# Kernel tuning notes

Measured on AMD Instinct MI355X. Metric: run time of the kernel, lower is better.

The kernel has to match this reference:

```python
import jax, jax.numpy as jnp
import numpy as np

B, H, W, C, NH, WS = 4, 128, 128, 128, 4, 8
N = WS * WS
HD = C // NH
SCALE = HD ** -0.5
MLP_H = 4 * C


def _rel_index():
    coords = np.stack(np.meshgrid(np.arange(WS), np.arange(WS), indexing='ij'))
    flat = coords.reshape(2, -1)
    rel = (flat[:, :, None] - flat[:, None, :]).transpose(1, 2, 0).astype(np.int64)
    rel[..., 0] += WS - 1
    rel[..., 1] += WS - 1
    rel[..., 0] *= 2 * WS - 1
    return jnp.asarray(rel.sum(-1))  # (N, N)

REL_IDX = _rel_index()


def layer_norm(x, w, b):
    m = jnp.mean(x, -1, keepdims=True)
    v = jnp.mean((x - m) ** 2, -1, keepdims=True)
    return (x - m) * jax.lax.rsqrt(v + 1e-5) * w + b


def window_partition(x):  # (B, H*W, C) -> (B*nW, N, C)
    t = x.reshape(B, H // WS, WS, W // WS, WS, C).transpose(0, 1, 3, 2, 4, 5)
    return t.reshape(-1, N, C)


def window_reverse(wins):  # (B*nW, N, C) -> (B, H*W, C)
    t = wins.reshape(B, H // WS, W // WS, WS, WS, C).transpose(0, 1, 3, 2, 4, 5)
    return t.reshape(B, H * W, C)


def setup_inputs():
    key = jax.random.key(0)
    ks = jax.random.split(key, 8)
    rn = lambda k, s: jax.random.normal(k, s, jnp.float32) * 0.02
    return {
        'x': jax.random.normal(ks[0], (B, H * W, C), jnp.float32),
        'd': jax.random.normal(ks[1], (B, H * W, C), jnp.float32),
        'rpb_table': rn(ks[2], ((2 * WS - 1) ** 2, NH)),
        'norm1_w': jnp.ones((C,), jnp.float32), 'norm1_b': jnp.zeros((C,), jnp.float32),
        'norm2_w': jnp.ones((C,), jnp.float32), 'norm2_b': jnp.zeros((C,), jnp.float32),
        'qkv1_w': rn(ks[3], (4 * C, C)), 'qkv1_b': jnp.zeros((4 * C,), jnp.float32),
        'proj_w': rn(ks[4], (C, C)), 'proj_b': jnp.zeros((C,), jnp.float32),
        'fc1_w': rn(ks[5], (MLP_H, C)), 'fc1_b': jnp.zeros((MLP_H,), jnp.float32),
        'fc2_w': rn(ks[6], (C, MLP_H)), 'fc2_b': jnp.zeros((C,), jnp.float32),
    }


def _attn_core(xw, dw, rpb_table, qkv1_w, qkv1_b, proj_w, proj_b):
    def qkv(t):
        q = (t @ qkv1_w.T + qkv1_b).reshape(-1, N, 4, NH, HD)
        return jnp.moveaxis(q, 2, 0).transpose(0, 1, 3, 2, 4)  # (4, B_, NH, N, HD)

    q_r, k_r, v_r, q_rd = qkv(xw)
    q_d, k_d, v_d, q_dr = qkv(dw)
    bias = rpb_table[REL_IDX].transpose(2, 0, 1)  # (NH, N, N)
    sm = jax.nn.softmax
    dot = lambda q, k: jnp.einsum('bhnd,bhmd->bhnm', q * SCALE, k)
    attn = sm(dot(q_r, k_r) + bias[None])      # bias only on r-branch (as in torch)
    attn_rd = sm(dot(q_dr, k_r))
    attn_d = sm(dot(q_d, k_d))
    attn_dr = sm(dot(q_rd, k_d))
    av = lambda a, v: jnp.einsum('bhnm,bhmd->bhnd', a, v).transpose(0, 2, 1, 3).reshape(-1, N, C)
    x_out = av(attn, v_r) + av(attn_rd, v_r)
    d_out = av(attn_dr, v_d) + av(attn_d, v_d)
    return x_out @ proj_w.T + proj_b, d_out @ proj_w.T + proj_b


def reference(x, d, rpb_table, norm1_w, norm1_b, norm2_w, norm2_b, qkv1_w, qkv1_b, proj_w, proj_b, fc1_w, fc1_b, fc2_w, fc2_b):
    xw = window_partition(layer_norm(x, norm1_w, norm1_b))
    dw = window_partition(layer_norm(d, norm1_w, norm1_b))
    xa, da = _attn_core(xw, dw, rpb_table, qkv1_w, qkv1_b, proj_w, proj_b)
    x = x + window_reverse(xa)
    d = d + window_reverse(da)
    mlp = lambda t: jax.nn.gelu(t @ fc1_w.T + fc1_b, approximate=False) @ fc2_w.T + fc2_b
    x = x + mlp(layer_norm(x, norm2_w, norm2_b))
    d = d + mlp(layer_norm(d, norm2_w, norm2_b))
    return x, d
```

## Files before the change

kernel.cpp:

```cpp
#include <hip/hip_runtime.h>
#include <hip/hip_bf16.h>
#include <math.h>

typedef short bf16x8 __attribute__((ext_vector_type(8)));
typedef float f32x4 __attribute__((ext_vector_type(4)));

#define QKSCALE_L2E 0.25505402227437564f
#define LOG2E 1.4426950408889634f

__device__ __forceinline__ unsigned short f2bf(float f) {
  __hip_bfloat16 h = __float2bfloat16(f);
  return *reinterpret_cast<unsigned short*>(&h);
}
__device__ __forceinline__ unsigned int pk2(float lo, float hi) {
  __hip_bfloat162 h = __float22bfloat162_rn(make_float2(lo, hi));
  return *reinterpret_cast<unsigned int*>(&h);
}
__device__ __forceinline__ bf16x8 pack8(const float* g) {
  union { unsigned int u[4]; bf16x8 v; } t;
  t.u[0] = pk2(g[0], g[1]); t.u[1] = pk2(g[2], g[3]);
  t.u[2] = pk2(g[4], g[5]); t.u[3] = pk2(g[6], g[7]);
  return t.v;
}

__device__ __forceinline__ bf16x8 ldsv(const unsigned short* base, int row, int strideHalfs, int kHalf, int swzMask) {
  int byte = row * strideHalfs * 2 + kHalf * 2;
  byte ^= (row & swzMask) << 4;
  return *(const bf16x8*)((const char*)base + byte);
}
__device__ __forceinline__ void ldss(unsigned short* base, int row, int strideHalfs, int col, int swzMask, unsigned short v) {
  int byte = row * strideHalfs * 2 + col * 2;
  byte ^= (row & swzMask) << 4;
  *(unsigned short*)((char*)base + byte) = v;
}
__device__ __forceinline__ void ldst32(unsigned short* base, int row, int strideHalfs, int colHalf, int swzMask, unsigned int v) {
  int byte = row * strideHalfs * 2 + colHalf * 2;
  byte ^= (row & swzMask) << 4;
  *(unsigned int*)((char*)base + byte) = v;
}
__device__ __forceinline__ void ldst64(unsigned short* base, int row, int strideHalfs, int colHalf, int swzMask, unsigned int lo, unsigned int hi) {
  int byte = row * strideHalfs * 2 + colHalf * 2;
  byte ^= (row & swzMask) << 4;
  uint2 val; val.x = lo; val.y = hi;
  *(uint2*)((char*)base + byte) = val;
}

__global__ void prep_kernel(
    const float* __restrict__ qkv1_w, const float* __restrict__ qkv1_b,
    const float* __restrict__ proj_w, const float* __restrict__ fc1_w,
    const float* __restrict__ fc2_w,  const float* __restrict__ rpb,
    unsigned short* __restrict__ Wqkvf, unsigned short* __restrict__ Wprojf,
    unsigned short* __restrict__ Wfc1f, unsigned short* __restrict__ Wfc2f,
    float* __restrict__ bqkv, float* __restrict__ biasmat)
{
  int i = blockIdx.x * 256 + threadIdx.x;
  if (i < 65536) {
    int j = i & 7, lane = (i >> 3) & 63, kk = (i >> 9) & 3;
    int sub16 = (i >> 11) & 1, h = (i >> 12) & 3, comp = i >> 14;
    int row = comp * 128 + h * 32 + sub16 * 16 + (lane & 15);
    int col = kk * 32 + (lane >> 4) * 8 + j;
    float sc = (comp == 0 || comp == 3) ? QKSCALE_L2E : 1.f;
    Wqkvf[i] = f2bf(qkv1_w[row * 128 + col] * sc);
  }
  int o = i - 65536;
  if (o >= 0 && o < 16384) {
    int j = o & 7, lane = (o >> 3) & 63, kk = (o >> 9) & 3, nf = o >> 11;
    int row = nf * 16 + (lane & 15);
    int cp = kk * 32 + (lane >> 4) * 8 + j;
    int H = cp >> 5, q = cp & 31, a = q >> 1, b = q & 1;
    Wprojf[o] = f2bf(proj_w[row * 128 + H * 32 + 16 * b + a]);
  }
  o -= 16384;
  if (o >= 0 && o < 65536) {
    int j = o & 7, lane = (o >> 3) & 63, kk = (o >> 9) & 3, n16 = o >> 11;
    int row = n16 * 16 + (lane & 15);
    int cp = kk * 32 + (lane >> 4) * 8 + j;
    Wfc1f[o] = f2bf(fc1_w[row * 128 + 16 * (cp & 7) + (cp >> 3)]);
  }
  o -= 65536;
  if (o >= 0 && o < 65536) {
    int j = o & 7, lane = (o >> 3) & 63, kk = (o >> 9) & 15, n8 = o >> 13;
    int row = n8 * 16 + (lane & 15);
    int m = kk * 32 + (lane >> 4) * 8 + j;
    int src = (m >> 6) * 64 + 16 * (m & 3) + ((m >> 2) & 15);
    Wfc2f[o] = f2bf(fc2_w[row * 512 + src]);
  }
  o -= 65536;
  if (o >= 0 && o < 512) {
    int comp = o >> 7;
    bqkv[o] = qkv1_b[o] * ((comp == 0 || comp == 3) ? QKSCALE_L2E : 1.f);
  }
  o -= 512;
  if (o >= 0 && o < 16384) {
    int hh = o >> 12, n = (o >> 6) & 63, m = o & 63;
    int di = (n >> 3) - (m >> 3) + 7, dj = (n & 7) - (m & 7) + 7;
    biasmat[o] = rpb[(di * 15 + dj) * 4 + hh] * LOG2E;
  }
}

__global__ void __launch_bounds__(256) ln1_kernel(
    const float* __restrict__ x_in, const float* __restrict__ d_in_,
    const float* __restrict__ n1w, const float* __restrict__ n1b,
    unsigned short* __restrict__ xg)
{
  const int s = blockIdx.x >> 10;
  const int row0 = (blockIdx.x & 1023) * 64;
  const int t = threadIdx.x >> 2, q4 = threadIdx.x & 3;
  const int grow = row0 + t;
  const int b2 = grow >> 14, rem = grow & 16383;
  const int gy = rem >> 7, gx = rem & 127;
  const int win = b2 * 256 + (gy >> 3) * 16 + (gx >> 3);
  const int tok = (gy & 7) * 8 + (gx & 7);
  const float* src = (s ? d_in_ : x_in) + (size_t)grow * 128 + q4 * 32;
  float v[32];
  float sum = 0.f, ss = 0.f;
#pragma unroll
  for (int i = 0; i < 8; ++i) {
    float4 f = ((const float4*)src)[i];
    v[i * 4 + 0] = f.x; v[i * 4 + 1] = f.y; v[i * 4 + 2] = f.z; v[i * 4 + 3] = f.w;
    sum += f.x + f.y + f.z + f.w;
    ss += f.x * f.x + f.y * f.y + f.z * f.z + f.w * f.w;
  }
  sum += __shfl_xor(sum, 1); sum += __shfl_xor(sum, 2);
  ss  += __shfl_xor(ss, 1);  ss  += __shfl_xor(ss, 2);
  float mean = sum * (1.f / 128.f);
  float var = ss * (1.f / 128.f) - mean * mean;
  float rs = rsqrtf(var + 1e-5f);
  unsigned short* base = xg + ((size_t)(s * 1024 + win)) * 8192
                         + ((tok >> 4) * 4 + q4) * 512 + (tok & 15) * 8;
#pragma unroll
  for (int i = 0; i < 4; ++i) {
    float g[8];
#pragma unroll
    for (int jj = 0; jj < 8; ++jj) {
      int c = q4 * 32 + i * 8 + jj;
      g[jj] = (v[i * 8 + jj] - mean) * rs * n1w[c] + n1b[c];
    }
    *(bf16x8*)(base + i * 128) = pack8(g);
  }
}

__global__ void __launch_bounds__(256, 4) attn_kernel(
    const unsigned short* __restrict__ xg,
    const unsigned short* __restrict__ Wqkvf, const float* __restrict__ bqkv,
    const float* __restrict__ biasmat,
    unsigned short* __restrict__ aout)
{
  __shared__ unsigned short smem[2][10240];

  const int tid = threadIdx.x, wid = tid >> 6, lane = tid & 63;
  const int l4 = lane >> 4, l15 = lane & 15;
  const int win = blockIdx.x & 1023, h = blockIdx.x >> 10;
  const f32x4 fzero = {0.f, 0.f, 0.f, 0.f};

  bf16x8 aF[2][4];
#pragma unroll
  for (int s = 0; s < 2; ++s) {
    const unsigned short* xw = xg + ((size_t)(s * 1024 + win)) * 8192;
#pragma unroll
    for (int kk = 0; kk < 4; ++kk)
      aF[s][kk] = *(const bf16x8*)(xw + (wid * 4 + kk) * 512 + lane * 8);
  }

  {
    f32x4 acc[2][8];
#pragma unroll
    for (int s = 0; s < 2; ++s)
#pragma unroll
      for (int n = 0; n < 8; ++n) acc[s][n] = fzero;
#pragma unroll
    for (int kk = 0; kk < 4; ++kk)
#pragma unroll
      for (int nf = 0; nf < 8; ++nf) {
        const int frag = (((nf >> 1) * 4 + h) * 2 + (nf & 1)) * 4 + kk;
        bf16x8 bb = *(const bf16x8*)(Wqkvf + frag * 512 + lane * 8);
        acc[0][nf] = __builtin_amdgcn_mfma_f32_16x16x32_bf16(aF[0][kk], bb, acc[0][nf], 0, 0, 0);
        acc[1][nf] = __builtin_amdgcn_mfma_f32_16x16x32_bf16(aF[1][kk], bb, acc[1][nf], 0, 0, 0);
      }
    float bv[8];
#pragma unroll
    for (int nf = 0; nf < 8; ++nf) bv[nf] = bqkv[(nf >> 1) * 128 + h * 32 + (nf & 1) * 16 + l15];
#pragma unroll
    for (int s = 0; s < 2; ++s)
#pragma unroll
      for (int r = 0; r < 4; ++r) {
        const int tw = wid * 16 + l4 * 4 + r;
        ldst32(smem[s] + 0,    tw, 32, 2 * l15, 3, pk2(acc[s][0][r] + bv[0], acc[s][1][r] + bv[1]));
        ldst32(smem[s] + 4096, tw, 32, 2 * l15, 3, pk2(acc[s][2][r] + bv[2], acc[s][3][r] + bv[3]));
        ldst32(smem[s] + 2048, tw, 32, 2 * l15, 3, pk2(acc[s][6][r] + bv[6], acc[s][7][r] + bv[7]));
        const int vc = 16 * l4 + 4 * r + wid;
        ldss(smem[s] + 8192, l15,      64, vc, 7, f2bf(acc[s][4][r] + bv[4]));
        ldss(smem[s] + 8192, 16 + l15, 64, vc, 7, f2bf(acc[s][5][r] + bv[5]));
      }
  }
  __syncthreads();

  const int s = wid >> 1, kind = wid & 1;
  bf16x8 aR[4], kR[4];
  {
    const unsigned short* Ab = kind ? (smem[1 - s] + 2048) : (smem[s] + 0);
    const unsigned short* Kb = smem[s] + 4096;
#pragma unroll
    for (int mf = 0; mf < 4; ++mf) aR[mf] = ldsv(Ab, mf * 16 + l15, 32, l4 * 8, 3);
#pragma unroll
    for (int nf = 0; nf < 4; ++nf) kR[nf] = ldsv(Kb, nf * 16 + l15, 32, l4 * 8, 3);
  }

  f32x4 sc[4][4];
#pragma unroll
  for (int mf = 0; mf < 4; ++mf)
#pragma unroll
    for (int nf = 0; nf < 4; ++nf) sc[mf][nf] = fzero;
#pragma unroll
  for (int mf = 0; mf < 4; ++mf)
#pragma unroll
    for (int nf = 0; nf < 4; ++nf)
      sc[mf][nf] = __builtin_amdgcn_mfma_f32_16x16x32_bf16(aR[mf], kR[nf], sc[mf][nf], 0, 0, 0);

  if (s == 0 && kind == 0) {
#pragma unroll
    for (int mf = 0; mf < 4; ++mf)
#pragma unroll
      for (int nf = 0; nf < 4; ++nf)
#pragma unroll
        for (int r = 0; r < 4; ++r) {
          int row = mf * 16 + l4 * 4 + r, col = nf * 16 + l15;
          sc[mf][nf][r] += biasmat[(h * 64 + row) * 64 + col];
        }
  }
#pragma unroll
  for (int mf = 0; mf < 4; ++mf) {
    float M = sc[mf][0][0];
#pragma unroll
    for (int nf = 0; nf < 4; ++nf)
#pragma unroll
      for (int r = 0; r < 4; ++r) M = fmaxf(M, sc[mf][nf][r]);
    M = fmaxf(M, __shfl_xor(M, 1));
    M = fmaxf(M, __shfl_xor(M, 2));
    M = fmaxf(M, __shfl_xor(M, 4));
    M = fmaxf(M, __shfl_xor(M, 8));
#pragma unroll
    for (int r = 0; r < 4; ++r) {
      float e0 = __builtin_amdgcn_exp2f(sc[mf][0][r] - M);
      float e1 = __builtin_amdgcn_exp2f(sc[mf][1][r] - M);
      float e2 = __builtin_amdgcn_exp2f(sc[mf][2][r] - M);
      float e3 = __builtin_amdgcn_exp2f(sc[mf][3][r] - M);
      float sm = e0 + e1 + e2 + e3;
      sm += __shfl_xor(sm, 1); sm += __shfl_xor(sm, 2);
      sm += __shfl_xor(sm, 4); sm += __shfl_xor(sm, 8);
      float inv = __builtin_amdgcn_rcpf(sm);
      sc[mf][0][r] = e0 * inv; sc[mf][1][r] = e1 * inv;
      sc[mf][2][r] = e2 * inv; sc[mf][3][r] = e3 * inv;
    }
  }
  __syncthreads();
  {
    unsigned short* Ptgt = smem[s] + (kind ? 4096 : 0);
#pragma unroll
    for (int mf = 0; mf < 4; ++mf)
#pragma unroll
      for (int r = 0; r < 4; ++r)
        ldst64(Ptgt, mf * 16 + l4 * 4 + r, 64, 4 * l15, 7,
               pk2(sc[mf][0][r], sc[mf][1][r]), pk2(sc[mf][2][r], sc[mf][3][r]));
  }
  __syncthreads();

  {
    const unsigned short* Vt = smem[s] + 8192;
    bf16x8 vR[2][2];
#pragma unroll
    for (int kk = 0; kk < 2; ++kk)
#pragma unroll
      for (int nf = 0; nf < 2; ++nf) vR[kk][nf] = ldsv(Vt, nf * 16 + l15, 64, kk * 32 + l4 * 8, 7);
    f32x4 pv[2][2];
    pv[0][0] = fzero; pv[0][1] = fzero; pv[1][0] = fzero; pv[1][1] = fzero;
#pragma unroll
    for (int pb_i = 0; pb_i < 2; ++pb_i) {
      const unsigned short* Pbuf = smem[s] + pb_i * 4096;
#pragma unroll
      for (int kk = 0; kk < 2; ++kk) {
        bf16x8 pa0 = ldsv(Pbuf, kind * 32 + l15, 64, kk * 32 + l4 * 8, 7);
        bf16x8 pa1 = ldsv(Pbuf, kind * 32 + 16 + l15, 64, kk * 32 + l4 * 8, 7);
#pragma unroll
        for (int nf = 0; nf < 2; ++nf) {
          pv[0][nf] = __builtin_amdgcn_mfma_f32_16x16x32_bf16(pa0, vR[kk][nf], pv[0][nf], 0, 0, 0);
          pv[1][nf] = __builtin_amdgcn_mfma_f32_16x16x32_bf16(pa1, vR[kk][nf], pv[1][nf], 0, 0, 0);
        }
      }
    }
#pragma unroll
    for (int mf = 0; mf < 2; ++mf)
#pragma unroll
      for (int r = 0; r < 4; ++r) {
        int tw = kind * 32 + mf * 16 + l4 * 4 + r;
        *(unsigned int*)(aout + ((size_t)s * 65536 + (size_t)win * 64 + tw) * 128 + h * 32 + 2 * l15) =
            pk2(pv[mf][0][r], pv[mf][1][r]);
      }
  }
}

__global__ void __launch_bounds__(256, 4) proj_kernel(
    const unsigned short* __restrict__ aout, const unsigned short* __restrict__ Wprojf,
    const float* __restrict__ projb,
    const float* __restrict__ x_in, const float* __restrict__ d_in_,
    const float* __restrict__ n2w, const float* __restrict__ n2b,
    float* __restrict__ out, unsigned short* __restrict__ xn2)
{
  const int tid = threadIdx.x, wid = tid >> 6, lane = tid & 63;
  const int l4 = lane >> 4, l15 = lane & 15;
  const int s = blockIdx.x >> 9, blk = blockIdx.x & 511;
  const int row0 = blk * 128 + wid * 32;
  const unsigned short* A = aout + (size_t)s * 65536 * 128;
  const f32x4 fzero = {0.f, 0.f, 0.f, 0.f};

  bf16x8 aF[2][4];
#pragma unroll
  for (int mf = 0; mf < 2; ++mf)
#pragma unroll
    for (int kk = 0; kk < 4; ++kk)
      aF[mf][kk] = *(const bf16x8*)(A + (size_t)(row0 + mf * 16 + l15) * 128 + kk * 32 + l4 * 8);

  f32x4 acc[2][8];
#pragma unroll
  for (int mf = 0; mf < 2; ++mf)
#pragma unroll
    for (int nf = 0; nf < 8; ++nf) acc[mf][nf] = fzero;
#pragma unroll
  for (int kk = 0; kk < 4; ++kk)
#pragma unroll
    for (int nf = 0; nf < 8; ++nf) {
      bf16x8 bb = *(const bf16x8*)(Wprojf + (nf * 4 + kk) * 512 + lane * 8);
      acc[0][nf] = __builtin_amdgcn_mfma_f32_16x16x32_bf16(aF[0][kk], bb, acc[0][nf], 0, 0, 0);
      acc[1][nf] = __builtin_amdgcn_mfma_f32_16x16x32_bf16(aF[1][kk], bb, acc[1][nf], 0, 0, 0);
    }

  float pbv[8], w2v[8], b2v[8];
#pragma unroll
  for (int nf = 0; nf < 8; ++nf) {
    int col = nf * 16 + l15;
    pbv[nf] = projb[col]; w2v[nf] = n2w[col]; b2v[nf] = n2b[col];
  }
  const float* resid = s ? d_in_ : x_in;
  float* dst = out + (size_t)s * 8388608;
#pragma unroll
  for (int mf = 0; mf < 2; ++mf)
#pragma unroll
    for (int r = 0; r < 4; ++r) {
      int t = row0 + mf * 16 + l4 * 4 + r;
      int w2 = t >> 6, tk = t & 63;
      int b2 = w2 >> 8, hb = (w2 >> 4) & 15, wb = w2 & 15;
      int grow = b2 * 16384 + hb * 1024 + (tk >> 3) * 128 + wb * 8 + (tk & 7);
      float v[8];
      float sum = 0.f, ssq = 0.f;
#pragma unroll
      for (int nf = 0; nf < 8; ++nf) {
        size_t off = (size_t)grow * 128 + nf * 16 + l15;
        float val = acc[mf][nf][r] + pbv[nf] + resid[off];
        v[nf] = val; sum += val; ssq += val * val;
        dst[off] = val;
      }
      sum += __shfl_xor(sum, 1); sum += __shfl_xor(sum, 2);
      sum += __shfl_xor(sum, 4); sum += __shfl_xor(sum, 8);
      ssq += __shfl_xor(ssq, 1); ssq += __shfl_xor(ssq, 2);
      ssq += __shfl_xor(ssq, 4); ssq += __shfl_xor(ssq, 8);
      float mean = sum * (1.f / 128.f);
      float var = ssq * (1.f / 128.f) - mean * mean;
      float rs = rsqrtf(var + 1e-5f);
      float g[8];
#pragma unroll
      for (int nf = 0; nf < 8; ++nf) g[nf] = (v[nf] - mean) * rs * w2v[nf] + b2v[nf];
      size_t fidx = ((size_t)s * 4096 + (grow >> 4)) * 4 + (l15 >> 2);
      *(bf16x8*)(xn2 + fidx * 512 + ((l15 & 3) * 16 + (grow & 15)) * 8) = pack8(g);
    }
}

__global__ void __launch_bounds__(512, 2) mlp_kernel(
    const unsigned short* __restrict__ xn2,
    const unsigned short* __restrict__ Wfc1f, const float* __restrict__ fc1b,
    const unsigned short* __restrict__ Wfc2f, const float* __restrict__ fc2b,
    float* __restrict__ out)
{
  __shared__ unsigned short hbuf[32 * 512];
  const int tid = threadIdx.x, wid = tid >> 6, lane = tid & 63;
  const int l4 = lane >> 4, l15 = lane & 15;
  const f32x4 fzero = {0.f, 0.f, 0.f, 0.f};

  bf16x8 wf1[16], wf2[16];
#pragma unroll
  for (int q = 0; q < 16; ++q)
    wf1[q] = *(const bf16x8*)(Wfc1f + (size_t)((wid * 4 + (q >> 2)) * 4 + (q & 3)) * 512 + lane * 8);
#pragma unroll
  for (int kk = 0; kk < 16; ++kk)
    wf2[kk] = *(const bf16x8*)(Wfc2f + (size_t)(wid * 16 + kk) * 512 + lane * 8);

  float b1v[4];
#pragma unroll
  for (int nf = 0; nf < 4; ++nf) b1v[nf] = fc1b[wid * 64 + nf * 16 + l15];
  const float b2c = fc2b[wid * 16 + l15];
  const int ocol = wid * 16 + l15;

  const size_t tokbase = (size_t)blockIdx.x * 512;

  for (int it = 0; it < 16; ++it) {
    if (it) __syncthreads();
    const size_t tb = tokbase + it * 32;
    f32x4 acc[2][4];
#pragma unroll
    for (int mf = 0; mf < 2; ++mf)
#pragma unroll
      for (int nf = 0; nf < 4; ++nf) acc[mf][nf] = fzero;
#pragma unroll
    for (int mf = 0; mf < 2; ++mf)
#pragma unroll
      for (int kk = 0; kk < 4; ++kk) {
        bf16x8 a = *(const bf16x8*)(xn2 + (((tb >> 4) + mf) * 4 + kk) * 512 + lane * 8);
#pragma unroll
        for (int nf = 0; nf < 4; ++nf)
          acc[mf][nf] = __builtin_amdgcn_mfma_f32_16x16x32_bf16(a, wf1[nf * 4 + kk], acc[mf][nf], 0, 0, 0);
      }
#pragma unroll
    for (int mf = 0; mf < 2; ++mf)
#pragma unroll
      for (int r = 0; r < 4; ++r) {
        float g[4];
#pragma unroll
        for (int nf = 0; nf < 4; ++nf) {
          float vv = acc[mf][nf][r] + b1v[nf];
          float x2 = vv * vv;
          float u2 = vv * fmaf(-0.10294455f, x2, -2.3022078f);
          float e = __builtin_amdgcn_exp2f(u2);
          g[nf] = vv * __builtin_amdgcn_rcpf(1.f + e);
        }
        ldst64(hbuf, mf * 16 + l4 * 4 + r, 512, wid * 64 + l15 * 4, 7,
               pk2(g[0], g[1]), pk2(g[2], g[3]));
      }
    __syncthreads();
    f32x4 a2[2];
    a2[0] = fzero; a2[1] = fzero;
#pragma unroll
    for (int kk = 0; kk < 16; ++kk) {
      bf16x8 h0 = ldsv(hbuf, l15, 512, kk * 32 + l4 * 8, 7);
      bf16x8 h1 = ldsv(hbuf, 16 + l15, 512, kk * 32 + l4 * 8, 7);
      a2[0] = __builtin_amdgcn_mfma_f32_16x16x32_bf16(h0, wf2[kk], a2[0], 0, 0, 0);
      a2[1] = __builtin_amdgcn_mfma_f32_16x16x32_bf16(h1, wf2[kk], a2[1], 0, 0, 0);
    }
#pragma unroll
    for (int mf = 0; mf < 2; ++mf)
#pragma unroll
      for (int r = 0; r < 4; ++r) {
        size_t off = (tb + mf * 16 + l4 * 4 + r) * 128 + ocol;
        out[off] = a2[mf][r] + b2c + out[off];
      }
  }
}

extern "C" void kernel_launch(void* const* d_in, const int* in_sizes, int n_in,
                              void* d_out, int out_size, void* d_ws, size_t ws_size,
                              hipStream_t stream) {
  const float* x    = (const float*)d_in[0];
  const float* dd   = (const float*)d_in[1];
  const float* rpb  = (const float*)d_in[2];
  const float* n1w  = (const float*)d_in[3];
  const float* n1b  = (const float*)d_in[4];
  const float* n2w  = (const float*)d_in[5];
  const float* n2b  = (const float*)d_in[6];
  const float* qkvw = (const float*)d_in[7];
  const float* qkvb = (const float*)d_in[8];
  const float* pw   = (const float*)d_in[9];
  const float* pb   = (const float*)d_in[10];
  const float* f1w  = (const float*)d_in[11];
  const float* f1b  = (const float*)d_in[12];
  const float* f2w  = (const float*)d_in[13];
  const float* f2b  = (const float*)d_in[14];
  float* out = (float*)d_out;
  char* ws = (char*)d_ws;
  unsigned short* Wqkvf  = (unsigned short*)(ws);
  unsigned short* Wprojf = (unsigned short*)(ws + 131072);
  unsigned short* Wfc1f  = (unsigned short*)(ws + 163840);
  unsigned short* Wfc2f  = (unsigned short*)(ws + 294912);
  float* bqkv            = (float*)(ws + 425984);
  float* biasmat         = (float*)(ws + 428032);
  unsigned short* aout   = (unsigned short*)(ws + 524288);
  unsigned short* xn2    = (unsigned short*)(ws + 524288 + 33554432);
  unsigned short* xg     = (unsigned short*)d_out;

  prep_kernel<<<dim3(899), dim3(256), 0, stream>>>(qkvw, qkvb, pw, f1w, f2w, rpb,
                                                   Wqkvf, Wprojf, Wfc1f, Wfc2f, bqkv, biasmat);
  ln1_kernel<<<dim3(2048), dim3(256), 0, stream>>>(x, dd, n1w, n1b, xg);
  attn_kernel<<<dim3(4096), dim3(256), 0, stream>>>(xg, Wqkvf, bqkv, biasmat, aout);
  proj_kernel<<<dim3(1024), dim3(256), 0, stream>>>(aout, Wprojf, pb, x, dd, n2w, n2b, out, xn2);
  mlp_kernel<<<dim3(256), dim3(512), 0, stream>>>(xn2, Wfc1f, f1b, Wfc2f, f2b, out);
}
```

Measured before the change: 210.7 us.

## Store post-attention residual as bf16 and retune the q/k LDS swizzle

proj_kernel now writes the post-attention residual stream as bf16, in window order, into the reused aout buffer instead of writing fp32 into the output. mlp_kernel gathers that residual back through the window-to-image index mapping, so the output is written once rather than read-modify-written. Separately, the q/k tiles in shared memory inside the attention kernel use a new XOR swizzle to change bank-conflict behaviour. The aim is to cut global memory traffic, at the cost of rounding the residual to bf16 and a less coalesced gathered read.

```diff
diff --git a/kernel.cpp b/kernel.cpp
--- a/kernel.cpp
+++ b/kernel.cpp
@@ -11,6 +11,9 @@
 __device__ __forceinline__ unsigned short f2bf(float f) {
   __hip_bfloat16 h = __float2bfloat16(f);
   return *reinterpret_cast<unsigned short*>(&h);
+}
+__device__ __forceinline__ float bf2f(unsigned short h) {
+  return __uint_as_float(((unsigned int)h) << 16);
 }
 __device__ __forceinline__ unsigned int pk2(float lo, float hi) {
   __hip_bfloat162 h = __float22bfloat162_rn(make_float2(lo, hi));
@@ -33,16 +36,21 @@
   byte ^= (row & swzMask) << 4;
   *(unsigned short*)((char*)base + byte) = v;
 }
-__device__ __forceinline__ void ldst32(unsigned short* base, int row, int strideHalfs, int colHalf, int swzMask, unsigned int v) {
-  int byte = row * strideHalfs * 2 + colHalf * 2;
-  byte ^= (row & swzMask) << 4;
-  *(unsigned int*)((char*)base + byte) = v;
-}
 __device__ __forceinline__ void ldst64(unsigned short* base, int row, int strideHalfs, int colHalf, int swzMask, unsigned int lo, unsigned int hi) {
   int byte = row * strideHalfs * 2 + colHalf * 2;
   byte ^= (row & swzMask) << 4;
   uint2 val; val.x = lo; val.y = hi;
   *(uint2*)((char*)base + byte) = val;
+}
+__device__ __forceinline__ void ldst32q(unsigned short* base, int row, int colHalf, unsigned int v) {
+  int byte = row * 64 + colHalf * 2;
+  byte ^= ((row >> 2) & 1) << 6;
+  *(unsigned int*)((char*)base + byte) = v;
+}
+__device__ __forceinline__ bf16x8 ldsvq(const unsigned short* base, int row, int kHalf) {
+  int byte = row * 64 + kHalf * 2;
+  byte ^= ((row >> 2) & 1) << 6;
+  return *(const bf16x8*)((const char*)base + byte);
 }
 
 __global__ void prep_kernel(
@@ -185,9 +193,9 @@
 #pragma unroll
       for (int r = 0; r < 4; ++r) {
         const int tw = wid * 16 + l4 * 4 + r;
-        ldst32(smem[s] + 0,    tw, 32, 2 * l15, 3, pk2(acc[s][0][r] + bv[0], acc[s][1][r] + bv[1]));
-        ldst32(smem[s] + 4096, tw, 32, 2 * l15, 3, pk2(acc[s][2][r] + bv[2], acc[s][3][r] + bv[3]));
-        ldst32(smem[s] + 2048, tw, 32, 2 * l15, 3, pk2(acc[s][6][r] + bv[6], acc[s][7][r] + bv[7]));
+        ldst32q(smem[s] + 0,    tw, 2 * l15, pk2(acc[s][0][r] + bv[0], acc[s][1][r] + bv[1]));
+        ldst32q(smem[s] + 4096, tw, 2 * l15, pk2(acc[s][2][r] + bv[2], acc[s][3][r] + bv[3]));
+        ldst32q(smem[s] + 2048, tw, 2 * l15, pk2(acc[s][6][r] + bv[6], acc[s][7][r] + bv[7]));
         const int vc = 16 * l4 + 4 * r + wid;
         ldss(smem[s] + 8192, l15,      64, vc, 7, f2bf(acc[s][4][r] + bv[4]));
         ldss(smem[s] + 8192, 16 + l15, 64, vc, 7, f2bf(acc[s][5][r] + bv[5]));
@@ -201,9 +209,9 @@
     const unsigned short* Ab = kind ? (smem[1 - s] + 2048) : (smem[s] + 0);
     const unsigned short* Kb = smem[s] + 4096;
 #pragma unroll
-    for (int mf = 0; mf < 4; ++mf) aR[mf] = ldsv(Ab, mf * 16 + l15, 32, l4 * 8, 3);
-#pragma unroll
-    for (int nf = 0; nf < 4; ++nf) kR[nf] = ldsv(Kb, nf * 16 + l15, 32, l4 * 8, 3);
+    for (int mf = 0; mf < 4; ++mf) aR[mf] = ldsvq(Ab, mf * 16 + l15, l4 * 8);
+#pragma unroll
+    for (int nf = 0; nf < 4; ++nf) kR[nf] = ldsvq(Kb, nf * 16 + l15, l4 * 8);
   }
 
   f32x4 sc[4][4];
@@ -304,7 +312,7 @@
     const float* __restrict__ projb,
     const float* __restrict__ x_in, const float* __restrict__ d_in_,
     const float* __restrict__ n2w, const float* __restrict__ n2b,
-    float* __restrict__ out, unsigned short* __restrict__ xn2)
+    unsigned short* __restrict__ xv, unsigned short* __restrict__ xn2)
 {
   const int tid = threadIdx.x, wid = tid >> 6, lane = tid & 63;
   const int l4 = lane >> 4, l15 = lane & 15;
@@ -341,7 +349,6 @@
     pbv[nf] = projb[col]; w2v[nf] = n2w[col]; b2v[nf] = n2b[col];
   }
   const float* resid = s ? d_in_ : x_in;
-  float* dst = out + (size_t)s * 8388608;
 #pragma unroll
   for (int mf = 0; mf < 2; ++mf)
 #pragma unroll
@@ -357,8 +364,10 @@
         size_t off = (size_t)grow * 128 + nf * 16 + l15;
         float val = acc[mf][nf][r] + pbv[nf] + resid[off];
         v[nf] = val; sum += val; ssq += val * val;
-        dst[off] = val;
-      }
+      }
+#pragma unroll
+      for (int nf = 0; nf < 8; ++nf)
+        xv[((size_t)s * 65536 + t) * 128 + nf * 16 + l15] = f2bf(v[nf]);
       sum += __shfl_xor(sum, 1); sum += __shfl_xor(sum, 2);
       sum += __shfl_xor(sum, 4); sum += __shfl_xor(sum, 8);
       ssq += __shfl_xor(ssq, 1); ssq += __shfl_xor(ssq, 2);
@@ -375,7 +384,7 @@
 }
 
 __global__ void __launch_bounds__(512, 2) mlp_kernel(
-    const unsigned short* __restrict__ xn2,
+    const unsigned short* __restrict__ xn2, const unsigned short* __restrict__ xv,
     const unsigned short* __restrict__ Wfc1f, const float* __restrict__ fc1b,
     const unsigned short* __restrict__ Wfc2f, const float* __restrict__ fc2b,
     float* __restrict__ out)
@@ -444,12 +453,19 @@
       a2[0] = __builtin_amdgcn_mfma_f32_16x16x32_bf16(h0, wf2[kk], a2[0], 0, 0, 0);
       a2[1] = __builtin_amdgcn_mfma_f32_16x16x32_bf16(h1, wf2[kk], a2[1], 0, 0, 0);
     }
+    const int gp = (int)(tb & 65535);
+    const int sloc = (int)(tb >> 16);
+    const int b2i = gp >> 14, gy = (gp >> 7) & 127, gxb = gp & 127;
+    const int tC = (b2i * 256 + (gy >> 3) * 16 + (gxb >> 3)) * 64 + (gy & 7) * 8;
 #pragma unroll
     for (int mf = 0; mf < 2; ++mf)
 #pragma unroll
       for (int r = 0; r < 4; ++r) {
-        size_t off = (tb + mf * 16 + l4 * 4 + r) * 128 + ocol;
-        out[off] = a2[mf][r] + b2c + out[off];
+        int row = mf * 16 + l4 * 4 + r;
+        int tloc = tC + (row >> 3) * 64 + (row & 7);
+        float res = bf2f(xv[((size_t)(sloc * 65536 + tloc)) * 128 + ocol]);
+        size_t off = (tb + row) * 128 + ocol;
+        out[off] = a2[mf][r] + b2c + res;
       }
   }
 }
@@ -483,11 +499,12 @@
   unsigned short* aout   = (unsigned short*)(ws + 524288);
   unsigned short* xn2    = (unsigned short*)(ws + 524288 + 33554432);
   unsigned short* xg     = (unsigned short*)d_out;
+  unsigned short* xv     = aout;
 
   prep_kernel<<<dim3(899), dim3(256), 0, stream>>>(qkvw, qkvb, pw, f1w, f2w, rpb,
                                                    Wqkvf, Wprojf, Wfc1f, Wfc2f, bqkv, biasmat);
   ln1_kernel<<<dim3(2048), dim3(256), 0, stream>>>(x, dd, n1w, n1b, xg);
   attn_kernel<<<dim3(4096), dim3(256), 0, stream>>>(xg, Wqkvf, bqkv, biasmat, aout);
-  proj_kernel<<<dim3(1024), dim3(256), 0, stream>>>(aout, Wprojf, pb, x, dd, n2w, n2b, out, xn2);
-  mlp_kernel<<<dim3(256), dim3(512), 0, stream>>>(xn2, Wfc1f, f1b, Wfc2f, f2b, out);
-}
+  proj_kernel<<<dim3(1024), dim3(256), 0, stream>>>(aout, Wprojf, pb, x, dd, n2w, n2b, xv, xn2);
+  mlp_kernel<<<dim3(256), dim3(512), 0, stream>>>(xn2, xv, Wfc1f, f1b, Wfc2f, f2b, out);
+}
```

After: 211.6 us. Within noise of the previous version (+0.4%).
